# Kernel tuning notes

Measured on AMD Instinct MI355X. Metric: run time of the kernel, lower is better.

The kernel has to match this reference:

```python
import jax, jax.numpy as jnp
import numpy as np

N = 50000
E = 500000
R = 8
IN_DIM = 128
HID = 128
NUM_CLASSES = 16
NUM_GRAPHS = 64


def setup_inputs() -> dict:
    key = jax.random.key(0)
    ks = jax.random.split(key, 12)
    x = jax.random.normal(ks[0], (N, IN_DIM), dtype=jnp.float32)
    edge_index = jax.random.randint(ks[1], (2, E), 0, N)
    edge_type = jax.random.randint(ks[2], (E,), 0, R)
    batch = jnp.sort(jax.random.randint(ks[3], (N,), 0, NUM_GRAPHS))
    s = 1.0 / np.sqrt(IN_DIM)
    W1 = jax.random.uniform(ks[4], (R, IN_DIM, HID), minval=-s, maxval=s, dtype=jnp.float32)
    root1 = jax.random.uniform(ks[5], (IN_DIM, HID), minval=-s, maxval=s, dtype=jnp.float32)
    b1 = jnp.zeros((HID,), jnp.float32)
    s2 = 1.0 / np.sqrt(HID)
    W2 = jax.random.uniform(ks[6], (R, HID, HID), minval=-s2, maxval=s2, dtype=jnp.float32)
    root2 = jax.random.uniform(ks[7], (HID, HID), minval=-s2, maxval=s2, dtype=jnp.float32)
    b2 = jnp.zeros((HID,), jnp.float32)
    linW = jax.random.uniform(ks[8], (HID, NUM_CLASSES), minval=-s2, maxval=s2, dtype=jnp.float32)
    linb = jnp.zeros((NUM_CLASSES,), jnp.float32)
    return {"x": x, "edge_index": edge_index, "edge_type": edge_type, "batch": batch,
            "W1": W1, "root1": root1, "b1": b1, "W2": W2, "root2": root2, "b2": b2,
            "linW": linW, "linb": linb}


def rgcn_conv(x, src, dst, rel, W, root, b):
    # Per-relation transform of ALL nodes once: [R, N, H] (avoids per-edge weight gather)
    xW = jnp.einsum('nd,rdh->rnh', x, W)
    msg = xW[rel, src]                      # [E, H] gather per edge
    # PyG RGCNConv default aggr='mean': mean over neighbors per (dst, relation)
    seg = dst * R + rel                     # composite segment id
    cnt = jax.ops.segment_sum(jnp.ones((msg.shape[0],), msg.dtype), seg, num_segments=N * R)
    norm = 1.0 / jnp.maximum(cnt, 1.0)
    msg = msg * norm[seg][:, None]
    agg = jax.ops.segment_sum(msg, dst, num_segments=N)  # sum over relations folds in
    return agg + x @ root + b


def global_mean_pool(x, batch):
    sums = jax.ops.segment_sum(x, batch, num_segments=NUM_GRAPHS)
    cnt = jax.ops.segment_sum(jnp.ones((x.shape[0],), x.dtype), batch, num_segments=NUM_GRAPHS)
    return sums / jnp.maximum(cnt, 1.0)[:, None]


def reference(x, edge_index, edge_type, batch, W1, root1, b1, W2, root2, b2, linW, linb):
    src, dst = edge_index[0], edge_index[1]
    h = jax.nn.relu(rgcn_conv(x, src, dst, edge_type, W1, root1, b1))
    h = jax.nn.relu(rgcn_conv(h, src, dst, edge_type, W2, root2, b2))
    pooled = global_mean_pool(h, batch)     # [G, HID]
    return pooled @ linW + linb             # [G, NUM_CLASSES]
```

## Files before the change

### kernel.cpp

```cpp
#include <hip/hip_runtime.h>
#include <hip/hip_bf16.h>
#include <stdint.h>

#define N_NODES 50000
#define N_EDGES 500000
#define R_REL 8
#define HID 128
#define KIN 128
#define KOUT 1152
#define NUM_GRAPHS 64
#define NUM_CLASSES 16

#define BN 32
#define LDA 1160
#define NKC 36
#define NBLK 1563

typedef __attribute__((ext_vector_type(8))) short bf16x8;
typedef __attribute__((ext_vector_type(4))) float f32x4;

__device__ __forceinline__ uint16_t f2bf(float f) {
  uint32_t u = __float_as_uint(f);
  u += 0x7FFFu + ((u >> 16) & 1u);
  return (uint16_t)(u >> 16);
}
__device__ __forceinline__ float bf2f(uint32_t b) {
  return __uint_as_float(b << 16);
}
__device__ __forceinline__ uint32_t pack2bf(float a, float b) {
  return (uint32_t)f2bf(a) | ((uint32_t)f2bf(b) << 16);
}

#define HIST_B 1954
#define BND_B 196
#define PW_B 576
#define CVT_B 3125
__global__ __launch_bounds__(256) void k_prep(const int* __restrict__ ei, const int* __restrict__ et,
                                              int* __restrict__ deg,
                                              const int* __restrict__ batch,
                                              int* __restrict__ gs, int* __restrict__ ge,
                                              const float* __restrict__ W1, const float* __restrict__ root1,
                                              uint16_t* __restrict__ Wf1,
                                              const float* __restrict__ W2, const float* __restrict__ root2,
                                              uint16_t* __restrict__ Wf2,
                                              const float* __restrict__ x, uint16_t* __restrict__ xb) {
  int b = blockIdx.x;
  if (b < HIST_B) {
    int i = b * 256 + threadIdx.x;
    if (i < N_EDGES) atomicAdd(&deg[ei[N_EDGES + i]], 1);
    return;
  }
  b -= HIST_B;
  if (b < BND_B) {
    int i = b * 256 + threadIdx.x;
    if (i < N_NODES) {
      int g = batch[i];
      if (i == 0) gs[g] = 0;
      else { int pg = batch[i - 1]; if (pg != g) { ge[pg] = i; gs[g] = i; } }
      if (i == N_NODES - 1) ge[g] = N_NODES;
    }
    return;
  }
  b -= BND_B;
  if (b < 2 * PW_B) {
    const float* W    = (b < PW_B) ? W1 : W2;
    const float* root = (b < PW_B) ? root1 : root2;
    uint16_t*    Wf   = (b < PW_B) ? Wf1 : Wf2;
    int idx = (b % PW_B) * 256 + threadIdx.x;
    int e = idx & 7, L = (idx >> 3) & 63, f = idx >> 9;
    int quad = L >> 4, l16 = L & 15;
    int nt = f & 7, kc = f >> 3;
    int kk = kc * 32 + quad * 8 + e;
    int s = kk >> 7, k = kk & 127;
    int col = nt * 16 + l16;
    float v = (s < R_REL) ? W[((size_t)s * KIN + k) * HID + col] : root[(size_t)k * HID + col];
    Wf[idx] = f2bf(v);
    return;
  }
  b -= 2 * PW_B;
  {
    int i = b * 256 + threadIdx.x;
    const float4* p = (const float4*)x + (size_t)i * 2;
    float4 a = p[0], c = p[1];
    uint4 o;
    o.x = pack2bf(a.x, a.y); o.y = pack2bf(a.z, a.w);
    o.z = pack2bf(c.x, c.y); o.w = pack2bf(c.z, c.w);
    *(uint4*)(xb + (size_t)i * 8) = o;
  }
}

__global__ __launch_bounds__(256) void k_scan1(const int* __restrict__ deg, int* __restrict__ offs,
                                               int* __restrict__ bsum) {
  __shared__ int sh[256];
  int t = threadIdx.x;
  int base = blockIdx.x * 1024 + t * 4;
  int v[4]; int s = 0;
  #pragma unroll
  for (int i = 0; i < 4; ++i) { int idx = base + i; v[i] = (idx < N_NODES) ? deg[idx] : 0; s += v[i]; }
  sh[t] = s;
  __syncthreads();
  for (int d = 1; d < 256; d <<= 1) {
    int add = (t >= d) ? sh[t - d] : 0;
    __syncthreads();
    sh[t] += add;
    __syncthreads();
  }
  int run = sh[t] - s;
  if (t == 255) bsum[blockIdx.x] = sh[255];
  #pragma unroll
  for (int i = 0; i < 4; ++i) { int idx = base + i; if (idx < N_NODES) offs[idx] = run; run += v[i]; }
}

__global__ __launch_bounds__(512) void k_scan2(int* __restrict__ bsum, int nb) {
  __shared__ int sh[512];
  int t = threadIdx.x;
  int v = (t < nb) ? bsum[t] : 0;
  sh[t] = v;
  __syncthreads();
  for (int d = 1; d < 512; d <<= 1) {
    int add = (t >= d) ? sh[t - d] : 0;
    __syncthreads();
    sh[t] += add;
    __syncthreads();
  }
  if (t < nb) bsum[t] = sh[t] - v;
}

__global__ __launch_bounds__(256) void k_scan3(int* __restrict__ offs, int* __restrict__ nxt,
                                               const int* __restrict__ bsum) {
  int i = blockIdx.x * 256 + threadIdx.x;
  if (i < N_NODES) {
    int o = offs[i] + bsum[i >> 10];
    offs[i] = o;
    nxt[i] = o;
  }
  if (i == 0) offs[N_NODES] = N_EDGES;
}

__global__ __launch_bounds__(256) void k_scatter(const int* __restrict__ ei, const int* __restrict__ et,
                                                 int* __restrict__ nxt, uint32_t* __restrict__ epack) {
  int i = blockIdx.x * 256 + threadIdx.x;
  if (i < N_EDGES) {
    int rel = et[i];
    int key = ei[N_EDGES + i];
    int p = atomicAdd(&nxt[key], 1);
    epack[p] = (uint32_t)ei[i] | ((uint32_t)rel << 16);
  }
}

template<int MODE>
__global__ __launch_bounds__(512, 4) void k_fused(const uint16_t* __restrict__ hin,
                                                  const uint32_t* __restrict__ epack,
                                                  const int* __restrict__ offs,
                                                  const uint16_t* __restrict__ Wf,
                                                  const float* __restrict__ bias,
                                                  void* __restrict__ hout,
                                                  float* __restrict__ psum,
                                                  const int* __restrict__ batch) {
  __shared__ __align__(16) uint16_t As[BN * LDA];
  int t = threadIdx.x;
  int w = __builtin_amdgcn_readfirstlane(t >> 6);
  int L = t & 63;
  int quad = L >> 4, l16 = L & 15;
  int node0 = blockIdx.x * BN;

  {
    bf16x8 z = 0;
    #pragma unroll
    for (int i = 0; i < 9; ++i) ((bf16x8*)As)[i * 512 + t] = z;
    if (t < 32) ((bf16x8*)As)[9 * 512 + t] = z;
  }

  int offv = offs[min(node0 + min(L, 32), N_NODES)];

  const uint16_t* wp = Wf + (size_t)w * 512 + (size_t)L * 8;
  bf16x8 b0 = *(const bf16x8*)(wp);
  bf16x8 b1 = *(const bf16x8*)(wp + 1 * 4096);
  bf16x8 b2 = *(const bf16x8*)(wp + 2 * 4096);
  bf16x8 b3 = *(const bf16x8*)(wp + 3 * 4096);

  __syncthreads();

  {
    #pragma unroll
    for (int ni = 0; ni < 4; ++ni) {
      int n = node0 + w * 4 + ni;
      if (n < N_NODES)
        *(uint32_t*)(As + (w * 4 + ni) * LDA + R_REL * HID + L * 2) =
            *(const uint32_t*)(hin + (size_t)n * HID + L * 2);
    }

    float ax[8] = {0,0,0,0,0,0,0,0}, ay[8] = {0,0,0,0,0,0,0,0};
    int cn[8] = {0,0,0,0,0,0,0,0};

    int o0   = __builtin_amdgcn_readlane(offv, w * 4);
    int oEnd = __builtin_amdgcn_readlane(offv, w * 4 + 4);
    int curb = 0;
    int nbound = __builtin_amdgcn_readlane(offv, w * 4 + 1);

    auto FLUSH = [&](int nl) {
      uint16_t* Ar = As + nl * LDA;
      #pragma unroll
      for (int r = 0; r < 8; ++r) {
        if (cn[r]) {
          float iv = 1.0f / (float)cn[r];
          *(uint32_t*)(Ar + r * HID + L * 2) = pack2bf(ax[r] * iv, ay[r] * iv);
          ax[r] = 0.f; ay[r] = 0.f; cn[r] = 0;
        }
      }
    };

    #pragma unroll 1
    for (int g = o0; g < oEnd; g += 16) {
      int m = min(16, oEnd - g);
      uint32_t pvv[16], sv[16], vv[16];
      #pragma unroll
      for (int i = 0; i < 16; ++i) if (i < m) pvv[i] = epack[g + i];
      #pragma unroll
      for (int i = 0; i < 16; ++i) if (i < m) {
        uint32_t ps = __builtin_amdgcn_readfirstlane(pvv[i]);
        sv[i] = ps;
        const uint16_t* bp = hin + (size_t)(ps & 0xFFFFu) * HID;
        vv[i] = *(const uint32_t*)(bp + 2u * (uint32_t)L);
      }
      #pragma unroll
      for (int i = 0; i < 16; ++i) if (i < m) {
        int e = g + i;
        while (e >= nbound) {
          FLUSH(w * 4 + curb);
          ++curb;
          nbound = __builtin_amdgcn_readlane(offv, w * 4 + curb + 1);
        }
        uint32_t v = vv[i];
        float lo = bf2f(v & 0xFFFFu), hi = bf2f(v >> 16);
        uint32_t r = sv[i] >> 16;
        if (r < 4) {
          if (r < 2) { if (r == 0) { ax[0]+=lo; ay[0]+=hi; ++cn[0]; } else { ax[1]+=lo; ay[1]+=hi; ++cn[1]; } }
          else       { if (r == 2) { ax[2]+=lo; ay[2]+=hi; ++cn[2]; } else { ax[3]+=lo; ay[3]+=hi; ++cn[3]; } }
        } else {
          if (r < 6) { if (r == 4) { ax[4]+=lo; ay[4]+=hi; ++cn[4]; } else { ax[5]+=lo; ay[5]+=hi; ++cn[5]; } }
          else       { if (r == 6) { ax[6]+=lo; ay[6]+=hi; ++cn[6]; } else { ax[7]+=lo; ay[7]+=hi; ++cn[7]; } }
        }
      }
    }
    FLUSH(w * 4 + curb);
  }
  __syncthreads();

  f32x4 acc0 = (f32x4){0.f, 0.f, 0.f, 0.f};
  f32x4 acc1 = (f32x4){0.f, 0.f, 0.f, 0.f};
  const uint16_t* ap = As + l16 * LDA + quad * 8;

  bf16x8 a0 = *(const bf16x8*)(ap);
  bf16x8 a1 = *(const bf16x8*)(ap + 16 * LDA);

  #pragma unroll 1
  for (int kc = 0; kc < 32; kc += 4) {
    bf16x8 n0, n1, nb;
    n0 = *(const bf16x8*)(ap + (kc + 1) * 32);
    n1 = *(const bf16x8*)(ap + (kc + 1) * 32 + 16 * LDA);
    nb = *(const bf16x8*)(wp + (size_t)(kc + 4) * 4096);
    acc0 = __builtin_amdgcn_mfma_f32_16x16x32_bf16(a0, b0, acc0, 0, 0, 0);
    acc1 = __builtin_amdgcn_mfma_f32_16x16x32_bf16(a1, b0, acc1, 0, 0, 0);
    a0 = n0; a1 = n1; b0 = nb;
    n0 = *(const bf16x8*)(ap + (kc + 2) * 32);
    n1 = *(const bf16x8*)(ap + (kc + 2) * 32 + 16 * LDA);
    nb = *(const bf16x8*)(wp + (size_t)(kc + 5) * 4096);
    acc0 = __builtin_amdgcn_mfma_f32_16x16x32_bf16(a0, b1, acc0, 0, 0, 0);
    acc1 = __builtin_amdgcn_mfma_f32_16x16x32_bf16(a1, b1, acc1, 0, 0, 0);
    a0 = n0; a1 = n1; b1 = nb;
    n0 = *(const bf16x8*)(ap + (kc + 3) * 32);
    n1 = *(const bf16x8*)(ap + (kc + 3) * 32 + 16 * LDA);
    nb = *(const bf16x8*)(wp + (size_t)(kc + 6) * 4096);
    acc0 = __builtin_amdgcn_mfma_f32_16x16x32_bf16(a0, b2, acc0, 0, 0, 0);
    acc1 = __builtin_amdgcn_mfma_f32_16x16x32_bf16(a1, b2, acc1, 0, 0, 0);
    a0 = n0; a1 = n1; b2 = nb;
    n0 = *(const bf16x8*)(ap + (kc + 4) * 32);
    n1 = *(const bf16x8*)(ap + (kc + 4) * 32 + 16 * LDA);
    nb = *(const bf16x8*)(wp + (size_t)(kc + 7) * 4096);
    acc0 = __builtin_amdgcn_mfma_f32_16x16x32_bf16(a0, b3, acc0, 0, 0, 0);
    acc1 = __builtin_amdgcn_mfma_f32_16x16x32_bf16(a1, b3, acc1, 0, 0, 0);
    a0 = n0; a1 = n1; b3 = nb;
  }
  {
    bf16x8 n0, n1;
    n0 = *(const bf16x8*)(ap + 33 * 32);
    n1 = *(const bf16x8*)(ap + 33 * 32 + 16 * LDA);
    acc0 = __builtin_amdgcn_mfma_f32_16x16x32_bf16(a0, b0, acc0, 0, 0, 0);
    acc1 = __builtin_amdgcn_mfma_f32_16x16x32_bf16(a1, b0, acc1, 0, 0, 0);
    a0 = n0; a1 = n1;
    n0 = *(const bf16x8*)(ap + 34 * 32);
    n1 = *(const bf16x8*)(ap + 34 * 32 + 16 * LDA);
    acc0 = __builtin_amdgcn_mfma_f32_16x16x32_bf16(a0, b1, acc0, 0, 0, 0);
    acc1 = __builtin_amdgcn_mfma_f32_16x16x32_bf16(a1, b1, acc1, 0, 0, 0);
    a0 = n0; a1 = n1;
    n0 = *(const bf16x8*)(ap + 35 * 32);
    n1 = *(const bf16x8*)(ap + 35 * 32 + 16 * LDA);
    acc0 = __builtin_amdgcn_mfma_f32_16x16x32_bf16(a0, b2, acc0, 0, 0, 0);
    acc1 = __builtin_amdgcn_mfma_f32_16x16x32_bf16(a1, b2, acc1, 0, 0, 0);
    a0 = n0; a1 = n1;
    acc0 = __builtin_amdgcn_mfma_f32_16x16x32_bf16(a0, b3, acc0, 0, 0, 0);
    acc1 = __builtin_amdgcn_mfma_f32_16x16x32_bf16(a1, b3, acc1, 0, 0, 0);
  }

  int col = w * 16 + l16;
  float bv = bias[col];
  if (MODE == 0) {
    #pragma unroll
    for (int rg = 0; rg < 4; ++rg) {
      int row = node0 + quad * 4 + rg;
      if (row < N_NODES)
        ((uint16_t*)hout)[(size_t)row * HID + col] = f2bf(fmaxf(acc0[rg] + bv, 0.f));
    }
    #pragma unroll
    for (int rg = 0; rg < 4; ++rg) {
      int row = node0 + 16 + quad * 4 + rg;
      if (row < N_NODES)
        ((uint16_t*)hout)[(size_t)row * HID + col] = f2bf(fmaxf(acc1[rg] + bv, 0.f));
    }
  } else {
    bool fast = false;
    int gA = 0;
    if (node0 + BN <= N_NODES) {
      gA = batch[node0];
      int gB = batch[node0 + BN - 1];
      fast = (gA == gB);
    }
    if (fast) {
      float s = 0.f;
      #pragma unroll
      for (int rg = 0; rg < 4; ++rg) s += fmaxf(acc0[rg] + bv, 0.f);
      #pragma unroll
      for (int rg = 0; rg < 4; ++rg) s += fmaxf(acc1[rg] + bv, 0.f);
      s += __shfl_xor(s, 16);
      s += __shfl_xor(s, 32);
      if (quad == 0) atomicAdd(&psum[gA * HID + col], s);
    } else {
      int gp = -1; float run = 0.f;
      #pragma unroll
      for (int k = 0; k < 8; ++k) {
        int rg = k & 3;
        int row = node0 + (k >> 2) * 16 + quad * 4 + rg;
        float v = (k < 4) ? acc0[rg] : acc1[rg];
        if (row < N_NODES) {
          int gg = batch[row];
          if (gg != gp) {
            if (gp >= 0) atomicAdd(&psum[gp * HID + col], run);
            run = 0.f; gp = gg;
          }
          run += fmaxf(v + bv, 0.f);
        }
      }
      if (gp >= 0) atomicAdd(&psum[gp * HID + col], run);
    }
  }
}

__global__ __launch_bounds__(1024) void k_final(const float* __restrict__ psum,
                                                const int* __restrict__ gs, const int* __restrict__ ge,
                                                const float* __restrict__ linW, const float* __restrict__ linb,
                                                float* __restrict__ out) {
  int i = threadIdx.x;
  int g = i >> 4, c = i & 15;
  float inv = 1.f / fmaxf((float)(ge[g] - gs[g]), 1.f);
  float s = 0.f;
  #pragma unroll 8
  for (int k = 0; k < HID; ++k) s += psum[g * HID + k] * linW[k * NUM_CLASSES + c];
  out[i] = s * inv + linb[c];
}

extern "C" void kernel_launch(void* const* d_in, const int* in_sizes, int n_in,
                              void* d_out, int out_size, void* d_ws, size_t ws_size,
                              hipStream_t stream) {
  const float* x     = (const float*)d_in[0];
  const int*   ei    = (const int*)d_in[1];
  const int*   et    = (const int*)d_in[2];
  const int*   batch = (const int*)d_in[3];
  const float* W1    = (const float*)d_in[4];
  const float* root1 = (const float*)d_in[5];
  const float* b1    = (const float*)d_in[6];
  const float* W2    = (const float*)d_in[7];
  const float* root2 = (const float*)d_in[8];
  const float* b2    = (const float*)d_in[9];
  const float* linW  = (const float*)d_in[10];
  const float* linb  = (const float*)d_in[11];
  float* out = (float*)d_out;

  char* ws = (char*)d_ws;
  size_t off = 0;
  auto alloc = [&](size_t bytes) -> char* {
    char* p = ws + off;
    off += (bytes + 255) & ~(size_t)255;
    return p;
  };
  int*      deg   = (int*)alloc((size_t)N_NODES * 4);
  int*      gb    = (int*)alloc(2 * NUM_GRAPHS * 4);
  float*    psum  = (float*)alloc((size_t)NUM_GRAPHS * HID * 4);
  size_t zbytes = (((size_t)N_NODES * 4 + 255) & ~(size_t)255) + 512 + (size_t)NUM_GRAPHS * HID * 4;
  int*      gs    = gb;
  int*      ge    = gb + NUM_GRAPHS;
  int*      offs  = (int*)alloc((size_t)(N_NODES + 1) * 4);
  int*      nxt   = (int*)alloc((size_t)N_NODES * 4);
  int*      bsum  = (int*)alloc(512 * 4);
  uint32_t* epack = (uint32_t*)alloc((size_t)N_EDGES * 4);
  uint16_t* Wf1   = (uint16_t*)alloc((size_t)KOUT * KIN * 2);
  uint16_t* Wf2   = (uint16_t*)alloc((size_t)KOUT * KIN * 2);
  uint16_t* xb    = (uint16_t*)alloc((size_t)N_NODES * HID * 2);
  uint16_t* h1b   = (uint16_t*)alloc((size_t)N_NODES * HID * 2);

  hipMemsetAsync(deg, 0, zbytes, stream);

  int nb = (N_NODES + 1023) / 1024;
  k_prep<<<HIST_B + BND_B + 2 * PW_B + CVT_B, 256, 0, stream>>>(
      ei, et, deg, batch, gs, ge, W1, root1, Wf1, W2, root2, Wf2, x, xb);
  k_scan1<<<nb, 256, 0, stream>>>(deg, offs, bsum);
  k_scan2<<<1, 512, 0, stream>>>(bsum, nb);
  k_scan3<<<(N_NODES + 255) / 256, 256, 0, stream>>>(offs, nxt, bsum);
  k_scatter<<<(N_EDGES + 255) / 256, 256, 0, stream>>>(ei, et, nxt, epack);

  k_fused<0><<<NBLK, 512, 0, stream>>>(xb,  epack, offs, Wf1, b1, h1b, nullptr, nullptr);
  k_fused<1><<<NBLK, 512, 0, stream>>>(h1b, epack, offs, Wf2, b2, nullptr, psum, batch);

  k_final<<<1, 1024, 0, stream>>>(psum, gs, ge, linW, linb, out);
}
```

Baseline: 316.7 us.

## Sort edges by (dst, relation) segment and balance gather work across waves

```diff
diff --git a/kernel.cpp b/kernel.cpp
--- a/kernel.cpp
+++ b/kernel.cpp
@@ -8,12 +8,12 @@
 #define HID 128
 #define KIN 128
 #define KOUT 1152
+#define N8 400000
 #define NUM_GRAPHS 64
 #define NUM_CLASSES 16
 
 #define BN 32
 #define LDA 1160
-#define NKC 36
 #define NBLK 1563
 
 typedef __attribute__((ext_vector_type(8))) short bf16x8;
@@ -30,13 +30,14 @@
 __device__ __forceinline__ uint32_t pack2bf(float a, float b) {
   return (uint32_t)f2bf(a) | ((uint32_t)f2bf(b) << 16);
 }
+#define MFMA(a, b, c) __builtin_amdgcn_mfma_f32_16x16x32_bf16((a), (b), (c), 0, 0, 0)
 
 #define HIST_B 1954
 #define BND_B 196
-#define PW_B 576
+#define WP_B 72
 #define CVT_B 3125
 __global__ __launch_bounds__(256) void k_prep(const int* __restrict__ ei, const int* __restrict__ et,
-                                              int* __restrict__ deg,
+                                              int* __restrict__ deg8,
                                               const int* __restrict__ batch,
                                               int* __restrict__ gs, int* __restrict__ ge,
                                               const float* __restrict__ W1, const float* __restrict__ root1,
@@ -45,14 +46,15 @@
                                               uint16_t* __restrict__ Wf2,
                                               const float* __restrict__ x, uint16_t* __restrict__ xb) {
   int b = blockIdx.x;
+  int t = threadIdx.x;
   if (b < HIST_B) {
-    int i = b * 256 + threadIdx.x;
-    if (i < N_EDGES) atomicAdd(&deg[ei[N_EDGES + i]], 1);
+    int i = b * 256 + t;
+    if (i < N_EDGES) atomicAdd(&deg8[ei[N_EDGES + i] * R_REL + et[i]], 1);
     return;
   }
   b -= HIST_B;
   if (b < BND_B) {
-    int i = b * 256 + threadIdx.x;
+    int i = b * 256 + t;
     if (i < N_NODES) {
       int g = batch[i];
       if (i == 0) gs[g] = 0;
@@ -62,24 +64,47 @@
     return;
   }
   b -= BND_B;
-  if (b < 2 * PW_B) {
-    const float* W    = (b < PW_B) ? W1 : W2;
-    const float* root = (b < PW_B) ? root1 : root2;
-    uint16_t*    Wf   = (b < PW_B) ? Wf1 : Wf2;
-    int idx = (b % PW_B) * 256 + threadIdx.x;
-    int e = idx & 7, L = (idx >> 3) & 63, f = idx >> 9;
-    int quad = L >> 4, l16 = L & 15;
-    int nt = f & 7, kc = f >> 3;
-    int kk = kc * 32 + quad * 8 + e;
-    int s = kk >> 7, k = kk & 127;
-    int col = nt * 16 + l16;
-    float v = (s < R_REL) ? W[((size_t)s * KIN + k) * HID + col] : root[(size_t)k * HID + col];
-    Wf[idx] = f2bf(v);
+  if (b < WP_B) {
+    __shared__ float lw[32 * 129];
+    const float* W    = (b < 36) ? W1 : W2;
+    const float* root = (b < 36) ? root1 : root2;
+    uint16_t*    Wf   = (b < 36) ? Wf1 : Wf2;
+    int kc = (b < 36) ? b : b - 36;
+    #pragma unroll
+    for (int j = 0; j < 4; ++j) {
+      int fi = j * 256 + t;
+      int row = fi >> 5, c4 = fi & 31;
+      int kk = kc * 32 + row;
+      int s = kk >> 7, k = kk & 127;
+      const float* src = (s < R_REL) ? (W + ((size_t)s * KIN + k) * HID) : (root + (size_t)k * HID);
+      float4 v = *(const float4*)(src + c4 * 4);
+      lw[row * 129 + c4 * 4 + 0] = v.x;
+      lw[row * 129 + c4 * 4 + 1] = v.y;
+      lw[row * 129 + c4 * 4 + 2] = v.z;
+      lw[row * 129 + c4 * 4 + 3] = v.w;
+    }
+    __syncthreads();
+    #pragma unroll
+    for (int p = 0; p < 2; ++p) {
+      int slot = p * 256 + t;
+      int nt = slot >> 6, L = slot & 63;
+      int quad = L >> 4, l16 = L & 15;
+      uint16_t tmp[8];
+      #pragma unroll
+      for (int e = 0; e < 8; ++e)
+        tmp[e] = f2bf(lw[(quad * 8 + e) * 129 + nt * 16 + l16]);
+      uint4 o;
+      o.x = (uint32_t)tmp[0] | ((uint32_t)tmp[1] << 16);
+      o.y = (uint32_t)tmp[2] | ((uint32_t)tmp[3] << 16);
+      o.z = (uint32_t)tmp[4] | ((uint32_t)tmp[5] << 16);
+      o.w = (uint32_t)tmp[6] | ((uint32_t)tmp[7] << 16);
+      *(uint4*)(Wf + ((size_t)(kc * 8 + nt) * 512 + (size_t)L * 8)) = o;
+    }
     return;
   }
-  b -= 2 * PW_B;
+  b -= WP_B;
   {
-    int i = b * 256 + threadIdx.x;
+    int i = b * 256 + t;
     const float4* p = (const float4*)x + (size_t)i * 2;
     float4 a = p[0], c = p[1];
     uint4 o;
@@ -89,14 +114,14 @@
   }
 }
 
-__global__ __launch_bounds__(256) void k_scan1(const int* __restrict__ deg, int* __restrict__ offs,
+__global__ __launch_bounds__(256) void k_scan1(const int* __restrict__ deg8, int* __restrict__ offs8,
                                                int* __restrict__ bsum) {
   __shared__ int sh[256];
   int t = threadIdx.x;
   int base = blockIdx.x * 1024 + t * 4;
   int v[4]; int s = 0;
   #pragma unroll
-  for (int i = 0; i < 4; ++i) { int idx = base + i; v[i] = (idx < N_NODES) ? deg[idx] : 0; s += v[i]; }
+  for (int i = 0; i < 4; ++i) { int idx = base + i; v[i] = (idx < N8) ? deg8[idx] : 0; s += v[i]; }
   sh[t] = s;
   __syncthreads();
   for (int d = 1; d < 256; d <<= 1) {
@@ -108,7 +133,7 @@
   int run = sh[t] - s;
   if (t == 255) bsum[blockIdx.x] = sh[255];
   #pragma unroll
-  for (int i = 0; i < 4; ++i) { int idx = base + i; if (idx < N_NODES) offs[idx] = run; run += v[i]; }
+  for (int i = 0; i < 4; ++i) { int idx = base + i; if (idx < N8) offs8[idx] = run; run += v[i]; }
 }
 
 __global__ __launch_bounds__(512) void k_scan2(int* __restrict__ bsum, int nb) {
@@ -126,15 +151,15 @@
   if (t < nb) bsum[t] = sh[t] - v;
 }
 
-__global__ __launch_bounds__(256) void k_scan3(int* __restrict__ offs, int* __restrict__ nxt,
+__global__ __launch_bounds__(256) void k_scan3(int* __restrict__ offs8, int* __restrict__ nxt,
                                                const int* __restrict__ bsum) {
   int i = blockIdx.x * 256 + threadIdx.x;
-  if (i < N_NODES) {
-    int o = offs[i] + bsum[i >> 10];
-    offs[i] = o;
+  if (i < N8) {
+    int o = offs8[i] + bsum[i >> 10];
+    offs8[i] = o;
     nxt[i] = o;
   }
-  if (i == 0) offs[N_NODES] = N_EDGES;
+  if (i == 0) offs8[N8] = N_EDGES;
 }
 
 __global__ __launch_bounds__(256) void k_scatter(const int* __restrict__ ei, const int* __restrict__ et,
@@ -142,16 +167,16 @@
   int i = blockIdx.x * 256 + threadIdx.x;
   if (i < N_EDGES) {
     int rel = et[i];
-    int key = ei[N_EDGES + i];
-    int p = atomicAdd(&nxt[key], 1);
-    epack[p] = (uint32_t)ei[i] | ((uint32_t)rel << 16);
+    int dst = ei[N_EDGES + i];
+    int p = atomicAdd(&nxt[dst * R_REL + rel], 1);
+    epack[p] = (uint32_t)ei[i] | ((uint32_t)rel << 16) | ((uint32_t)(dst & 31) << 19);
   }
 }
 
 template<int MODE>
 __global__ __launch_bounds__(512, 4) void k_fused(const uint16_t* __restrict__ hin,
                                                   const uint32_t* __restrict__ epack,
-                                                  const int* __restrict__ offs,
+                                                  const int* __restrict__ offs8,
                                                   const uint16_t* __restrict__ Wf,
                                                   const float* __restrict__ bias,
                                                   void* __restrict__ hout,
@@ -163,6 +188,7 @@
   int L = t & 63;
   int quad = L >> 4, l16 = L & 15;
   int node0 = blockIdx.x * BN;
+  int voff = 2 * L;
 
   {
     bf16x8 z = 0;
@@ -171,8 +197,6 @@
     if (t < 32) ((bf16x8*)As)[9 * 512 + t] = z;
   }
 
-  int offv = offs[min(node0 + min(L, 32), N_NODES)];
-
   const uint16_t* wp = Wf + (size_t)w * 512 + (size_t)L * 8;
   bf16x8 b0 = *(const bf16x8*)(wp);
   bf16x8 b1 = *(const bf16x8*)(wp + 1 * 4096);
@@ -181,69 +205,65 @@
 
   __syncthreads();
 
+  #pragma unroll
+  for (int ni = 0; ni < 4; ++ni) {
+    int r = w * 4 + ni;
+    int n = node0 + r;
+    if (n < N_NODES)
+      *(uint32_t*)(As + (size_t)r * LDA + R_REL * HID + voff) =
+          *(const uint32_t*)(hin + (size_t)n * HID + voff);
+  }
+
   {
-    #pragma unroll
-    for (int ni = 0; ni < 4; ++ni) {
-      int n = node0 + w * 4 + ni;
-      if (n < N_NODES)
-        *(uint32_t*)(As + (w * 4 + ni) * LDA + R_REL * HID + L * 2) =
-            *(const uint32_t*)(hin + (size_t)n * HID + L * 2);
-    }
-
-    float ax[8] = {0,0,0,0,0,0,0,0}, ay[8] = {0,0,0,0,0,0,0,0};
-    int cn[8] = {0,0,0,0,0,0,0,0};
-
-    int o0   = __builtin_amdgcn_readlane(offv, w * 4);
-    int oEnd = __builtin_amdgcn_readlane(offv, w * 4 + 4);
-    int curb = 0;
-    int nbound = __builtin_amdgcn_readlane(offv, w * 4 + 1);
-
-    auto FLUSH = [&](int nl) {
-      uint16_t* Ar = As + nl * LDA;
-      #pragma unroll
-      for (int r = 0; r < 8; ++r) {
-        if (cn[r]) {
-          float iv = 1.0f / (float)cn[r];
-          *(uint32_t*)(Ar + r * HID + L * 2) = pack2bf(ax[r] * iv, ay[r] * iv);
-          ax[r] = 0.f; ay[r] = 0.f; cn[r] = 0;
+    int s0 = offs8[(size_t)node0 * R_REL];
+    int s1 = offs8[(size_t)min(node0 + BN, N_NODES) * R_REL];
+    int ce = s1 - s0;
+    int e0 = s0 + ((ce * w) >> 3);
+    int e1 = s0 + ((ce * (w + 1)) >> 3);
+    uint32_t kskip = 0xFFFFFFFEu;
+    if (e0 > s0) kskip = epack[e0 - 1] >> 16;
+    uint32_t cur = 0xFFFFFFFFu;
+    float ax = 0.f, ay = 0.f; int ct = 0;
+    bool done = false;
+    int lsel = L & 15;
+    uint32_t pv = (e0 < s1) ? epack[e0 + lsel] : 0u;
+    #pragma unroll 1
+    for (int g = e0; g < s1 && !done; g += 16) {
+      uint32_t pc = pv;
+      int m = min(16, s1 - g);
+      pv = epack[g + 16 + lsel];
+      uint32_t sv[16], vv[16];
+      #pragma unroll
+      for (int i = 0; i < 16; ++i) if (i < m) {
+        uint32_t s = (uint32_t)__builtin_amdgcn_readlane((int)pc, i);
+        sv[i] = s;
+        vv[i] = *(const uint32_t*)(hin + (size_t)(s & 0xFFFFu) * HID + voff);
+      }
+      #pragma unroll
+      for (int i = 0; i < 16; ++i) {
+        if (i >= m) break;
+        uint32_t k = sv[i] >> 16;
+        if (k == cur) {
+          uint32_t v = vv[i];
+          ax += bf2f(v & 0xFFFFu); ay += bf2f(v >> 16); ++ct;
+        } else if (k != kskip) {
+          if (cur != 0xFFFFFFFFu) {
+            float iv = __builtin_amdgcn_rcpf((float)ct);
+            *(uint32_t*)(As + (size_t)(cur >> 3) * LDA + (cur & 7u) * HID + voff) =
+                pack2bf(ax * iv, ay * iv);
+          }
+          if (g + i >= e1) { done = true; cur = 0xFFFFFFFFu; break; }
+          cur = k;
+          uint32_t v = vv[i];
+          ax = bf2f(v & 0xFFFFu); ay = bf2f(v >> 16); ct = 1;
         }
       }
-    };
-
-    #pragma unroll 1
-    for (int g = o0; g < oEnd; g += 16) {
-      int m = min(16, oEnd - g);
-      uint32_t pvv[16], sv[16], vv[16];
-      #pragma unroll
-      for (int i = 0; i < 16; ++i) if (i < m) pvv[i] = epack[g + i];
-      #pragma unroll
-      for (int i = 0; i < 16; ++i) if (i < m) {
-        uint32_t ps = __builtin_amdgcn_readfirstlane(pvv[i]);
-        sv[i] = ps;
-        const uint16_t* bp = hin + (size_t)(ps & 0xFFFFu) * HID;
-        vv[i] = *(const uint32_t*)(bp + 2u * (uint32_t)L);
-      }
-      #pragma unroll
-      for (int i = 0; i < 16; ++i) if (i < m) {
-        int e = g + i;
-        while (e >= nbound) {
-          FLUSH(w * 4 + curb);
-          ++curb;
-          nbound = __builtin_amdgcn_readlane(offv, w * 4 + curb + 1);
-        }
-        uint32_t v = vv[i];
-        float lo = bf2f(v & 0xFFFFu), hi = bf2f(v >> 16);
-        uint32_t r = sv[i] >> 16;
-        if (r < 4) {
-          if (r < 2) { if (r == 0) { ax[0]+=lo; ay[0]+=hi; ++cn[0]; } else { ax[1]+=lo; ay[1]+=hi; ++cn[1]; } }
-          else       { if (r == 2) { ax[2]+=lo; ay[2]+=hi; ++cn[2]; } else { ax[3]+=lo; ay[3]+=hi; ++cn[3]; } }
-        } else {
-          if (r < 6) { if (r == 4) { ax[4]+=lo; ay[4]+=hi; ++cn[4]; } else { ax[5]+=lo; ay[5]+=hi; ++cn[5]; } }
-          else       { if (r == 6) { ax[6]+=lo; ay[6]+=hi; ++cn[6]; } else { ax[7]+=lo; ay[7]+=hi; ++cn[7]; } }
-        }
-      }
-    }
-    FLUSH(w * 4 + curb);
+    }
+    if (cur != 0xFFFFFFFFu) {
+      float iv = __builtin_amdgcn_rcpf((float)ct);
+      *(uint32_t*)(As + (size_t)(cur >> 3) * LDA + (cur & 7u) * HID + voff) =
+          pack2bf(ax * iv, ay * iv);
+    }
   }
   __syncthreads();
 
@@ -260,47 +280,47 @@
     n0 = *(const bf16x8*)(ap + (kc + 1) * 32);
     n1 = *(const bf16x8*)(ap + (kc + 1) * 32 + 16 * LDA);
     nb = *(const bf16x8*)(wp + (size_t)(kc + 4) * 4096);
-    acc0 = __builtin_amdgcn_mfma_f32_16x16x32_bf16(a0, b0, acc0, 0, 0, 0);
-    acc1 = __builtin_amdgcn_mfma_f32_16x16x32_bf16(a1, b0, acc1, 0, 0, 0);
+    acc0 = MFMA(a0, b0, acc0);
+    acc1 = MFMA(a1, b0, acc1);
     a0 = n0; a1 = n1; b0 = nb;
     n0 = *(const bf16x8*)(ap + (kc + 2) * 32);
     n1 = *(const bf16x8*)(ap + (kc + 2) * 32 + 16 * LDA);
     nb = *(const bf16x8*)(wp + (size_t)(kc + 5) * 4096);
-    acc0 = __builtin_amdgcn_mfma_f32_16x16x32_bf16(a0, b1, acc0, 0, 0, 0);
-    acc1 = __builtin_amdgcn_mfma_f32_16x16x32_bf16(a1, b1, acc1, 0, 0, 0);
+    acc0 = MFMA(a0, b1, acc0);
+    acc1 = MFMA(a1, b1, acc1);
     a0 = n0; a1 = n1; b1 = nb;
     n0 = *(const bf16x8*)(ap + (kc + 3) * 32);
     n1 = *(const bf16x8*)(ap + (kc + 3) * 32 + 16 * LDA);
     nb = *(const bf16x8*)(wp + (size_t)(kc + 6) * 4096);
-    acc0 = __builtin_amdgcn_mfma_f32_16x16x32_bf16(a0, b2, acc0, 0, 0, 0);
-    acc1 = __builtin_amdgcn_mfma_f32_16x16x32_bf16(a1, b2, acc1, 0, 0, 0);
+    acc0 = MFMA(a0, b2, acc0);
+    acc1 = MFMA(a1, b2, acc1);
     a0 = n0; a1 = n1; b2 = nb;
     n0 = *(const bf16x8*)(ap + (kc + 4) * 32);
     n1 = *(const bf16x8*)(ap + (kc + 4) * 32 + 16 * LDA);
     nb = *(const bf16x8*)(wp + (size_t)(kc + 7) * 4096);
-    acc0 = __builtin_amdgcn_mfma_f32_16x16x32_bf16(a0, b3, acc0, 0, 0, 0);
-    acc1 = __builtin_amdgcn_mfma_f32_16x16x32_bf16(a1, b3, acc1, 0, 0, 0);
+    acc0 = MFMA(a0, b3, acc0);
+    acc1 = MFMA(a1, b3, acc1);
     a0 = n0; a1 = n1; b3 = nb;
   }
   {
     bf16x8 n0, n1;
     n0 = *(const bf16x8*)(ap + 33 * 32);
     n1 = *(const bf16x8*)(ap + 33 * 32 + 16 * LDA);
-    acc0 = __builtin_amdgcn_mfma_f32_16x16x32_bf16(a0, b0, acc0, 0, 0, 0);
-    acc1 = __builtin_amdgcn_mfma_f32_16x16x32_bf16(a1, b0, acc1, 0, 0, 0);
+    acc0 = MFMA(a0, b0, acc0);
+    acc1 = MFMA(a1, b0, acc1);
     a0 = n0; a1 = n1;
     n0 = *(const bf16x8*)(ap + 34 * 32);
     n1 = *(const bf16x8*)(ap + 34 * 32 + 16 * LDA);
-    acc0 = __builtin_amdgcn_mfma_f32_16x16x32_bf16(a0, b1, acc0, 0, 0, 0);
-    acc1 = __builtin_amdgcn_mfma_f32_16x16x32_bf16(a1, b1, acc1, 0, 0, 0);
+    acc0 = MFMA(a0, b1, acc0);
+    acc1 = MFMA(a1, b1, acc1);
     a0 = n0; a1 = n1;
     n0 = *(const bf16x8*)(ap + 35 * 32);
     n1 = *(const bf16x8*)(ap + 35 * 32 + 16 * LDA);
-    acc0 = __builtin_amdgcn_mfma_f32_16x16x32_bf16(a0, b2, acc0, 0, 0, 0);
-    acc1 = __builtin_amdgcn_mfma_f32_16x16x32_bf16(a1, b2, acc1, 0, 0, 0);
+    acc0 = MFMA(a0, b2, acc0);
+    acc1 = MFMA(a1, b2, acc1);
     a0 = n0; a1 = n1;
-    acc0 = __builtin_amdgcn_mfma_f32_16x16x32_bf16(a0, b3, acc0, 0, 0, 0);
-    acc1 = __builtin_amdgcn_mfma_f32_16x16x32_bf16(a1, b3, acc1, 0, 0, 0);
+    acc0 = MFMA(a0, b3, acc0);
+    acc1 = MFMA(a1, b3, acc1);
   }
 
   int col = w * 16 + l16;
@@ -360,12 +380,19 @@
                                                 const int* __restrict__ gs, const int* __restrict__ ge,
                                                 const float* __restrict__ linW, const float* __restrict__ linb,
                                                 float* __restrict__ out) {
+  __shared__ float lp[NUM_GRAPHS * HID];
+  __shared__ float lw[HID * NUM_CLASSES];
   int i = threadIdx.x;
+  #pragma unroll
+  for (int j = 0; j < 8; ++j) lp[j * 1024 + i] = psum[j * 1024 + i];
+  #pragma unroll
+  for (int j = 0; j < 2; ++j) lw[j * 1024 + i] = linW[j * 1024 + i];
+  __syncthreads();
   int g = i >> 4, c = i & 15;
   float inv = 1.f / fmaxf((float)(ge[g] - gs[g]), 1.f);
   float s = 0.f;
   #pragma unroll 8
-  for (int k = 0; k < HID; ++k) s += psum[g * HID + k] * linW[k * NUM_CLASSES + c];
+  for (int k = 0; k < HID; ++k) s += lp[g * HID + k] * lw[k * NUM_CLASSES + c];
   out[i] = s * inv + linb[c];
 }
 
@@ -393,33 +420,33 @@
     off += (bytes + 255) & ~(size_t)255;
     return p;
   };
-  int*      deg   = (int*)alloc((size_t)N_NODES * 4);
+  int*      deg8  = (int*)alloc((size_t)N8 * 4);
   int*      gb    = (int*)alloc(2 * NUM_GRAPHS * 4);
   float*    psum  = (float*)alloc((size_t)NUM_GRAPHS * HID * 4);
-  size_t zbytes = (((size_t)N_NODES * 4 + 255) & ~(size_t)255) + 512 + (size_t)NUM_GRAPHS * HID * 4;
+  size_t zbytes = (size_t)N8 * 4 + 512 + (size_t)NUM_GRAPHS * HID * 4;
   int*      gs    = gb;
   int*      ge    = gb + NUM_GRAPHS;
-  int*      offs  = (int*)alloc((size_t)(N_NODES + 1) * 4);
-  int*      nxt   = (int*)alloc((size_t)N_NODES * 4);
+  int*      offs8 = (int*)alloc((size_t)(N8 + 1) * 4);
+  int*      nxt   = (int*)alloc((size_t)N8 * 4);
   int*      bsum  = (int*)alloc(512 * 4);
-  uint32_t* epack = (uint32_t*)alloc((size_t)N_EDGES * 4);
+  uint32_t* epack = (uint32_t*)alloc((size_t)(N_EDGES + 64) * 4);
   uint16_t* Wf1   = (uint16_t*)alloc((size_t)KOUT * KIN * 2);
   uint16_t* Wf2   = (uint16_t*)alloc((size_t)KOUT * KIN * 2);
   uint16_t* xb    = (uint16_t*)alloc((size_t)N_NODES * HID * 2);
   uint16_t* h1b   = (uint16_t*)alloc((size_t)N_NODES * HID * 2);
 
-  hipMemsetAsync(deg, 0, zbytes, stream);
-
-  int nb = (N_NODES + 1023) / 1024;
-  k_prep<<<HIST_B + BND_B + 2 * PW_B + CVT_B, 256, 0, stream>>>(
-      ei, et, deg, batch, gs, ge, W1, root1, Wf1, W2, root2, Wf2, x, xb);
-  k_scan1<<<nb, 256, 0, stream>>>(deg, offs, bsum);
+  hipMemsetAsync(deg8, 0, zbytes, stream);
+
+  int nb = (N8 + 1023) / 1024;
+  k_prep<<<HIST_B + BND_B + WP_B + CVT_B, 256, 0, stream>>>(
+      ei, et, deg8, batch, gs, ge, W1, root1, Wf1, W2, root2, Wf2, x, xb);
+  k_scan1<<<nb, 256, 0, stream>>>(deg8, offs8, bsum);
   k_scan2<<<1, 512, 0, stream>>>(bsum, nb);
-  k_scan3<<<(N_NODES + 255) / 256, 256, 0, stream>>>(offs, nxt, bsum);
+  k_scan3<<<(N8 + 255) / 256, 256, 0, stream>>>(offs8, nxt, bsum);
   k_scatter<<<(N_EDGES + 255) / 256, 256, 0, stream>>>(ei, et, nxt, epack);
 
-  k_fused<0><<<NBLK, 512, 0, stream>>>(xb,  epack, offs, Wf1, b1, h1b, nullptr, nullptr);
-  k_fused<1><<<NBLK, 512, 0, stream>>>(h1b, epack, offs, Wf2, b2, nullptr, psum, batch);
+  k_fused<0><<<NBLK, 512, 0, stream>>>(xb,  epack, offs8, Wf1, b1, h1b, nullptr, nullptr);
+  k_fused<1><<<NBLK, 512, 0, stream>>>(h1b, epack, offs8, Wf2, b2, nullptr, psum, batch);
 
   k_final<<<1, 1024, 0, stream>>>(psum, gs, ge, linW, linb, out);
 }
```

Measured after the change: 312.7 us. Within noise of the previous version (-1.3%).
